# Kernel optimization log

Measured on AMD Instinct MI355X. Metric: run time of the kernel, lower is better.

The kernel has to match this reference:

```python
import jax, jax.numpy as jnp
import numpy as np

TOP_K = 2
ROUTE_SCALE = 1.0
EPS = 1e-20

B, S, D = 2, 512, 1024
E = 8            # num_experts
F = 768          # moe_intermediate_size
FS = 768 * 1     # shared expert intermediate (moe_intermediate_size * num_shared_experts)


def setup_inputs() -> dict:
    key = jax.random.key(0)
    ks = jax.random.split(key, 9)
    s = 0.02
    return {
        "hidden_states": jax.random.normal(ks[0], (B, S, D), dtype=jnp.float32),
        "W_gate_router": jax.random.normal(ks[1], (D, E), dtype=jnp.float32) * s,
        "expert_bias": jnp.zeros((E,), dtype=jnp.float32),
        "Wg": jax.random.normal(ks[2], (E, D, F), dtype=jnp.float32) * s,
        "Wu": jax.random.normal(ks[3], (E, D, F), dtype=jnp.float32) * s,
        "Wd": jax.random.normal(ks[4], (E, F, D), dtype=jnp.float32) * s,
        "Wg_s": jax.random.normal(ks[5], (D, FS), dtype=jnp.float32) * s,
        "Wu_s": jax.random.normal(ks[6], (D, FS), dtype=jnp.float32) * s,
        "Wd_s": jax.random.normal(ks[7], (FS, D), dtype=jnp.float32) * s,
    }


def reference(hidden_states, W_gate_router, expert_bias, Wg, Wu, Wd, Wg_s, Wu_s, Wd_s):
    b, s, d = hidden_states.shape
    x = hidden_states.reshape(-1, d)                      # [T, D]
    T = x.shape[0]

    # ---- token-choice top-k router (sigmoid scoring, route_norm) ----
    logits = x @ W_gate_router                            # [T, E]
    scores = jax.nn.sigmoid(logits.astype(jnp.float32))   # [T, E] fp32
    _, sel = jax.lax.top_k(scores + expert_bias, TOP_K)   # [T, K] (bias only for selection)
    top_scores = jnp.take_along_axis(scores, sel, axis=1)  # [T, K]
    top_scores = top_scores / (top_scores.sum(-1, keepdims=True) + EPS)  # route_norm
    top_scores = top_scores * ROUTE_SCALE

    # ---- shared expert (always active) ----
    shared = (jax.nn.silu(x @ Wg_s) * (x @ Wu_s)) @ Wd_s  # [T, D]

    # ---- dispatch: N = T*K routed slots (scatter-add is order-independent,
    #      so the torch stable-argsort grouping is mathematically a no-op) ----
    tok = jnp.repeat(jnp.arange(T), TOP_K)                # [N] source token per slot
    exp = sel.reshape(-1)                                 # [N] expert per slot
    w = top_scores.reshape(-1)                            # [N]
    xr = x[tok]                                           # [N, D]

    # per-expert SiLU-GLU MLP, vectorized over experts then select own expert's row
    h = jax.nn.silu(jnp.einsum('nd,edf->enf', xr, Wg)) * jnp.einsum('nd,edf->enf', xr, Wu)
    out_all = jnp.einsum('enf,efd->end', h, Wd)           # [E, N, D]
    routed = out_all[exp, jnp.arange(exp.shape[0])]       # [N, D]
    routed = (routed.astype(jnp.float32) * w[:, None]).astype(hidden_states.dtype)

    # ---- combine: scatter-add routed outputs onto shared output ----
    out = shared.at[tok].add(routed)                      # [T, D]
    return out.reshape(b, s, d)
```

## Files before the change

kernel.cpp:

```cpp
#include <hip/hip_runtime.h>
#include <hip/hip_bf16.h>
#include <math.h>

#define T_TOK   1024
#define D_DIM   1024
#define E_NUM   8
#define F_DIM   768
#define N_SLOTS 2048

typedef unsigned short u16;
typedef __attribute__((ext_vector_type(8))) short bf16x8;
typedef __attribute__((ext_vector_type(4))) float f32x4;

#define WS_SEL    0
#define WS_WTS    8192
#define WS_BUCKET 16384
#define WS_COUNTS 49152
#define WS_OFFS   49216
#define WS_POS    49280
#define WS_XB     65536
#define WS_P1     (WS_XB + 2097152)
#define WS_H      (WS_P1 + 9437184)
#define WS_WDT    (WS_H + 4718592)
#define WS_WDST   (WS_WDT + 12582912)
#define WS_WGUT   (WS_WDST + 1572864)
#define WS_WGUST  (WS_WGUT + 25165824)
#define WS_Y      WS_WGUT

__device__ __forceinline__ u16 f2bf(float x) {
    unsigned int u = __float_as_uint(x);
    u += 0x7fffu + ((u >> 16) & 1u);
    return (u16)(u >> 16);
}
__device__ __forceinline__ float bf2f(u16 h) {
    return __uint_as_float(((unsigned int)h) << 16);
}

__device__ __forceinline__ void async16(const void* g, void* s) {
    __builtin_amdgcn_global_load_lds(
        (const __attribute__((address_space(1))) unsigned int*)g,
        (__attribute__((address_space(3))) unsigned int*)s, 16, 0, 0);
}

#define PIN()   __builtin_amdgcn_sched_barrier(0)
#define BAR()   do { PIN(); __builtin_amdgcn_s_barrier(); PIN(); } while (0)
#define WAIT6() do { asm volatile("s_waitcnt vmcnt(6)" ::: "memory"); PIN(); } while (0)
#define WAIT0() do { asm volatile("s_waitcnt vmcnt(0)" ::: "memory"); PIN(); } while (0)

__global__ __launch_bounds__(256) void router_kernel(
    const float* __restrict__ X, const float* __restrict__ Wr,
    const float* __restrict__ bias, int* __restrict__ sel, float* __restrict__ wts)
{
    int t = blockIdx.x * 4 + (threadIdx.x >> 6);
    int lane = threadIdx.x & 63;
    if (t >= T_TOK) return;
    const float* xrow = X + (size_t)t * D_DIM;
    float acc[E_NUM];
#pragma unroll
    for (int e = 0; e < E_NUM; ++e) acc[e] = 0.f;
    for (int d = lane; d < D_DIM; d += 64) {
        float xv = xrow[d];
        const float4* wr = (const float4*)(Wr + (size_t)d * E_NUM);
        float4 w0 = wr[0], w1 = wr[1];
        acc[0] += xv * w0.x; acc[1] += xv * w0.y; acc[2] += xv * w0.z; acc[3] += xv * w0.w;
        acc[4] += xv * w1.x; acc[5] += xv * w1.y; acc[6] += xv * w1.z; acc[7] += xv * w1.w;
    }
#pragma unroll
    for (int e = 0; e < E_NUM; ++e)
#pragma unroll
        for (int off = 32; off > 0; off >>= 1)
            acc[e] += __shfl_xor(acc[e], off);
    if (lane == 0) {
        float s[E_NUM], b[E_NUM];
#pragma unroll
        for (int e = 0; e < E_NUM; ++e) {
            s[e] = 1.f / (1.f + expf(-acc[e]));
            b[e] = s[e] + bias[e];
        }
        int i1 = 0; float b1 = b[0];
#pragma unroll
        for (int e = 1; e < E_NUM; ++e) if (b[e] > b1) { b1 = b[e]; i1 = e; }
        int i2 = -1; float b2 = -INFINITY;
#pragma unroll
        for (int e = 0; e < E_NUM; ++e) {
            if (e == i1) continue;
            if (b[e] > b2) { b2 = b[e]; i2 = e; }
        }
        float s1 = s[i1], s2 = s[i2];
        float denom = s1 + s2 + 1e-20f;
        sel[2 * t] = i1; sel[2 * t + 1] = i2;
        wts[2 * t] = s1 / denom; wts[2 * t + 1] = s2 / denom;
    }
}

__global__ __launch_bounds__(512) void dispatch_kernel(
    const int* __restrict__ sel, int* __restrict__ bucket,
    int* __restrict__ counts, int* __restrict__ offs, int* __restrict__ pos)
{
    __shared__ int soffs[E_NUM + 1];
    int e = threadIdx.x >> 6;
    int lane = threadIdx.x & 63;
    int running = 0;
    for (int base = 0; base < N_SLOTS; base += 64) {
        int slot = base + lane;
        bool mine = (sel[slot] == e);
        unsigned long long mask = __ballot(mine);
        if (mine) {
            int rank = running + __popcll(mask & ((1ull << lane) - 1ull));
            bucket[e * T_TOK + rank] = slot;
        }
        running += __popcll(mask);
    }
    if (lane == 0) counts[e] = running;
    __syncthreads();
    if (threadIdx.x == 0) {
        int o = 0;
        for (int k = 0; k < E_NUM; ++k) { soffs[k] = o; offs[k] = o; o += counts[k]; }
        soffs[E_NUM] = o; offs[E_NUM] = o;
    }
    __syncthreads();
    int base_off = soffs[e];
    for (int r = lane; r < running; r += 64)
        pos[bucket[e * T_TOK + r]] = base_off + r;
}

__global__ __launch_bounds__(256) void transpose_cvt(
    const float* __restrict__ Wg, const float* __restrict__ Wu,
    const float* __restrict__ Wd, const float* __restrict__ Wgs,
    const float* __restrict__ Wus, const float* __restrict__ Wds,
    u16* __restrict__ Wgut, u16* __restrict__ Wdt,
    u16* __restrict__ Wgust, u16* __restrict__ Wdst)
{
    int z = blockIdx.z;
    const float* src; u16* dst; int R, C;
    if (z < 8)       { src = Wg + (size_t)z * D_DIM * F_DIM;        dst = Wgut + (size_t)z * 1536 * D_DIM;               R = D_DIM; C = F_DIM; }
    else if (z < 16) { int e = z - 8;  src = Wu + (size_t)e * D_DIM * F_DIM; dst = Wgut + (size_t)e * 1536 * D_DIM + (size_t)F_DIM * D_DIM; R = D_DIM; C = F_DIM; }
    else if (z < 24) { int e = z - 16; src = Wd + (size_t)e * F_DIM * D_DIM; dst = Wdt + (size_t)e * D_DIM * F_DIM;      R = F_DIM; C = D_DIM; }
    else if (z == 24){ src = Wgs; dst = Wgust;                      R = D_DIM; C = F_DIM; }
    else if (z == 25){ src = Wus; dst = Wgust + (size_t)F_DIM * D_DIM; R = D_DIM; C = F_DIM; }
    else             { src = Wds; dst = Wdst;                       R = F_DIM; C = D_DIM; }
    int c0 = blockIdx.x * 64, r0 = blockIdx.y * 64;
    if (c0 >= C || r0 >= R) return;

    __shared__ u16 tile[64][72];
    int t = threadIdx.x;
    int rr = t >> 4, cq = (t & 15) * 4;
#pragma unroll
    for (int i = 0; i < 4; ++i) {
        int rl = rr + 16 * i;
        float4 v = *(const float4*)(src + (size_t)(r0 + rl) * C + c0 + cq);
        tile[cq + 0][rl] = f2bf(v.x);
        tile[cq + 1][rl] = f2bf(v.y);
        tile[cq + 2][rl] = f2bf(v.z);
        tile[cq + 3][rl] = f2bf(v.w);
    }
    __syncthreads();
#pragma unroll
    for (int j = 0; j < 2; ++j) {
        int idx = t + 256 * j;
        int cc = idx >> 3, q = idx & 7;
        *(uint4*)(dst + (size_t)(c0 + cc) * R + r0 + q * 8) = *(const uint4*)&tile[cc][q * 8];
    }
}

__global__ __launch_bounds__(256) void xcvt_kernel(
    const float* __restrict__ X, u16* __restrict__ Xb)
{
    int i8 = (blockIdx.x * 256 + threadIdx.x) * 8;
    float4 v0 = *(const float4*)(X + i8);
    float4 v1 = *(const float4*)(X + i8 + 4);
    u16 o[8];
    o[0] = f2bf(v0.x); o[1] = f2bf(v0.y); o[2] = f2bf(v0.z); o[3] = f2bf(v0.w);
    o[4] = f2bf(v1.x); o[5] = f2bf(v1.y); o[6] = f2bf(v1.z); o[7] = f2bf(v1.w);
    *(uint4*)(Xb + i8) = *(const uint4*)o;
}

__global__ __launch_bounds__(256, 3) void proj1(
    const u16* __restrict__ Xb, const u16* __restrict__ Wgut, const u16* __restrict__ Wgust,
    u16* __restrict__ P1,
    const int* __restrict__ bucket, const int* __restrict__ counts, const int* __restrict__ offs)
{
    const int i = blockIdx.x;
    const int cxcd = i & 7, m = i >> 3;
    const int y = m & 15, phi = m >> 4;
    const int panel = phi * 8 + cxcd;
    const int unit = panel / 24, x = panel - unit * 24;

    int nrows, rbase; const u16* Wt;
    if (unit < E_NUM) {
        nrows = counts[unit]; rbase = offs[unit];
        Wt = Wgut + (size_t)unit * 1536 * D_DIM;
    } else {
        nrows = T_TOK; rbase = N_SLOTS; Wt = Wgust;
    }
    const int row0 = y * 128, n0 = x * 64;
    if (row0 >= nrows) return;

    __shared__ u16 smem[2][192 * 64];

    const int t = threadIdx.x;
    const int wv = t >> 6, lane = t & 63, l15 = lane & 15, lg = lane >> 4;
    const int wm = wv >> 1, wn = wv & 1;
    const int rl = lane >> 3, cch = lane & 7;

    const u16* srcA[4];
#pragma unroll
    for (int j = 0; j < 4; ++j) {
        int arow = wv * 32 + j * 8 + rl;
        int grow = min(row0 + arow, nrows - 1);
        if (unit < E_NUM) grow = bucket[unit * T_TOK + grow] >> 1;
        srcA[j] = Xb + (size_t)grow * D_DIM + (cch ^ (arow & 7)) * 8;
    }
    const u16* srcB[2];
#pragma unroll
    for (int j = 0; j < 2; ++j) {
        int brow = wv * 16 + j * 8 + rl;
        srcB[j] = Wt + (size_t)(n0 + brow) * D_DIM + (cch ^ (brow & 7)) * 8;
    }

    f32x4 acc[4][2];
    const f32x4 z4 = {0.f, 0.f, 0.f, 0.f};
#pragma unroll
    for (int ri = 0; ri < 4; ++ri)
#pragma unroll
        for (int ci = 0; ci < 2; ++ci) acc[ri][ci] = z4;

#define STAGE1(buf, kt) do { \
    _Pragma("unroll") \
    for (int j = 0; j < 4; ++j) \
        async16(srcA[j] + (kt), &smem[buf][(wv * 32 + j * 8) * 64]); \
    _Pragma("unroll") \
    for (int j = 0; j < 2; ++j) \
        async16(srcB[j] + (kt), &smem[buf][(128 + wv * 16 + j * 8) * 64]); \
} while (0)

#define COMP1(buf) do { \
    bf16x8 av[4][2], bv[2][2]; \
    _Pragma("unroll") \
    for (int ri = 0; ri < 4; ++ri) { \
        int row = wm * 64 + ri * 16 + l15; \
        _Pragma("unroll") \
        for (int kk = 0; kk < 2; ++kk) { \
            int ch = ((kk << 2) | lg) ^ (row & 7); \
            av[ri][kk] = *(const bf16x8*)&smem[buf][row * 64 + ch * 8]; \
        } \
    } \
    _Pragma("unroll") \
    for (int ci = 0; ci < 2; ++ci) { \
        int br = wn * 32 + ci * 16 + l15; \
        _Pragma("unroll") \
        for (int kk = 0; kk < 2; ++kk) { \
            int ch = ((kk << 2) | lg) ^ (br & 7); \
            bv[ci][kk] = *(const bf16x8*)&smem[buf][(128 + br) * 64 + ch * 8]; \
        } \
    } \
    _Pragma("unroll") \
    for (int kk = 0; kk < 2; ++kk) \
        _Pragma("unroll") \
        for (int ri = 0; ri < 4; ++ri) \
            _Pragma("unroll") \
            for (int ci = 0; ci < 2; ++ci) \
                acc[ri][ci] = __builtin_amdgcn_mfma_f32_16x16x32_bf16( \
                    av[ri][kk], bv[ci][kk], acc[ri][ci], 0, 0, 0); \
} while (0)

    STAGE1(0, 0);
    for (int tt = 0; tt < 16; tt += 2) {
        STAGE1(1, (tt + 1) * 64);
        WAIT6();
        BAR();
        COMP1(0);
        BAR();
        if (tt + 2 < 16) { STAGE1(0, (tt + 2) * 64); WAIT6(); }
        else             { WAIT0(); }
        BAR();
        COMP1(1);
        BAR();
    }
#undef STAGE1
#undef COMP1

#pragma unroll
    for (int ri = 0; ri < 4; ++ri)
#pragma unroll
        for (int ci = 0; ci < 2; ++ci) {
            int n = n0 + wn * 32 + ci * 16 + l15;
#pragma unroll
            for (int r = 0; r < 4; ++r) {
                int row = row0 + wm * 64 + ri * 16 + lg * 4 + r;
                if (row >= nrows) continue;
                P1[(size_t)(rbase + row) * 1536 + n] = f2bf(acc[ri][ci][r]);
            }
        }
}

__global__ __launch_bounds__(256) void glu_kernel(
    const u16* __restrict__ P1, u16* __restrict__ H)
{
    int i8 = (blockIdx.x * 256 + threadIdx.x) * 8;
    int r = i8 / F_DIM, f = i8 - r * F_DIM;
    bf16x8 g8 = *(const bf16x8*)(P1 + (size_t)r * 1536 + f);
    bf16x8 u8 = *(const bf16x8*)(P1 + (size_t)r * 1536 + F_DIM + f);
    u16 hv[8];
#pragma unroll
    for (int j = 0; j < 8; ++j) {
        float gv = bf2f((u16)g8[j]);
        float uv = bf2f((u16)u8[j]);
        hv[j] = f2bf(gv / (1.f + __expf(-gv)) * uv);
    }
    *(uint4*)(H + (size_t)r * F_DIM + f) = *(const uint4*)hv;
}

__global__ __launch_bounds__(256, 3) void proj2(
    const u16* __restrict__ H, const u16* __restrict__ Wdt, const u16* __restrict__ Wdst,
    float* __restrict__ Y,
    const int* __restrict__ counts, const int* __restrict__ offs)
{
    const int i = blockIdx.x;
    const int cxcd = i & 7, m = i >> 3;
    const int y = m & 15, phi = m >> 4;
    const int panel = phi * 8 + cxcd;
    const int unit = panel >> 4, x = panel & 15;

    int nrows, rbase; const u16* Wt;
    if (unit < E_NUM) {
        nrows = counts[unit]; rbase = offs[unit];
        Wt = Wdt + (size_t)unit * D_DIM * F_DIM;
    } else {
        nrows = T_TOK; rbase = N_SLOTS; Wt = Wdst;
    }
    const int row0 = y * 128, n0 = x * 64;
    if (row0 >= nrows) return;

    __shared__ u16 smem[2][192 * 64];

    const int t = threadIdx.x;
    const int wv = t >> 6, lane = t & 63, l15 = lane & 15, lg = lane >> 4;
    const int wm = wv >> 1, wn = wv & 1;
    const int rl = lane >> 3, cch = lane & 7;

    const u16* srcA[4];
#pragma unroll
    for (int j = 0; j < 4; ++j) {
        int arow = wv * 32 + j * 8 + rl;
        int grow = rbase + min(row0 + arow, nrows - 1);
        srcA[j] = H + (size_t)grow * F_DIM + (cch ^ (arow & 7)) * 8;
    }
    const u16* srcB[2];
#pragma unroll
    for (int j = 0; j < 2; ++j) {
        int brow = wv * 16 + j * 8 + rl;
        srcB[j] = Wt + (size_t)(n0 + brow) * F_DIM + (cch ^ (brow & 7)) * 8;
    }

    f32x4 acc[4][2];
    const f32x4 z4 = {0.f, 0.f, 0.f, 0.f};
#pragma unroll
    for (int ri = 0; ri < 4; ++ri)
#pragma unroll
        for (int ci = 0; ci < 2; ++ci) acc[ri][ci] = z4;

#define STAGE2(buf, kt) do { \
    _Pragma("unroll") \
    for (int j = 0; j < 4; ++j) \
        async16(srcA[j] + (kt), &smem[buf][(wv * 32 + j * 8) * 64]); \
    _Pragma("unroll") \
    for (int j = 0; j < 2; ++j) \
        async16(srcB[j] + (kt), &smem[buf][(128 + wv * 16 + j * 8) * 64]); \
} while (0)

#define COMP2(buf) do { \
    bf16x8 av[4][2], bv[2][2]; \
    _Pragma("unroll") \
    for (int ri = 0; ri < 4; ++ri) { \
        int row = wm * 64 + ri * 16 + l15; \
        _Pragma("unroll") \
        for (int kk = 0; kk < 2; ++kk) { \
            int ch = ((kk << 2) | lg) ^ (row & 7); \
            av[ri][kk] = *(const bf16x8*)&smem[buf][row * 64 + ch * 8]; \
        } \
    } \
    _Pragma("unroll") \
    for (int ci = 0; ci < 2; ++ci) { \
        int br = wn * 32 + ci * 16 + l15; \
        _Pragma("unroll") \
        for (int kk = 0; kk < 2; ++kk) { \
            int ch = ((kk << 2) | lg) ^ (br & 7); \
            bv[ci][kk] = *(const bf16x8*)&smem[buf][(128 + br) * 64 + ch * 8]; \
        } \
    } \
    _Pragma("unroll") \
    for (int kk = 0; kk < 2; ++kk) \
        _Pragma("unroll") \
        for (int ri = 0; ri < 4; ++ri) \
            _Pragma("unroll") \
            for (int ci = 0; ci < 2; ++ci) \
                acc[ri][ci] = __builtin_amdgcn_mfma_f32_16x16x32_bf16( \
                    av[ri][kk], bv[ci][kk], acc[ri][ci], 0, 0, 0); \
} while (0)

    STAGE2(0, 0);
    for (int tt = 0; tt < 12; tt += 2) {
        STAGE2(1, (tt + 1) * 64);
        WAIT6();
        BAR();
        COMP2(0);
        BAR();
        if (tt + 2 < 12) { STAGE2(0, (tt + 2) * 64); WAIT6(); }
        else             { WAIT0(); }
        BAR();
        COMP2(1);
        BAR();
    }
#undef STAGE2
#undef COMP2

#pragma unroll
    for (int ri = 0; ri < 4; ++ri)
#pragma unroll
        for (int ci = 0; ci < 2; ++ci) {
            int n = n0 + wn * 32 + ci * 16 + l15;
#pragma unroll
            for (int r = 0; r < 4; ++r) {
                int row = row0 + wm * 64 + ri * 16 + lg * 4 + r;
                if (row >= nrows) continue;
                Y[(size_t)(rbase + row) * D_DIM + n] = acc[ri][ci][r];
            }
        }
}

__global__ __launch_bounds__(256) void combine_kernel(
    const float* __restrict__ Y, const int* __restrict__ pos,
    const float* __restrict__ wts, float* __restrict__ out)
{
    int t = blockIdx.x;
    int d = threadIdx.x * 4;
    int p0 = pos[2 * t], p1 = pos[2 * t + 1];
    float w0 = wts[2 * t], w1 = wts[2 * t + 1];
    float4 a = *(const float4*)(Y + (size_t)(N_SLOTS + t) * D_DIM + d);
    float4 b = *(const float4*)(Y + (size_t)p0 * D_DIM + d);
    float4 cc = *(const float4*)(Y + (size_t)p1 * D_DIM + d);
    float4 o;
    o.x = a.x + w0 * b.x + w1 * cc.x;
    o.y = a.y + w0 * b.y + w1 * cc.y;
    o.z = a.z + w0 * b.z + w1 * cc.z;
    o.w = a.w + w0 * b.w + w1 * cc.w;
    *(float4*)(out + (size_t)t * D_DIM + d) = o;
}

extern "C" void kernel_launch(void* const* d_in, const int* in_sizes, int n_in,
                              void* d_out, int out_size, void* d_ws, size_t ws_size,
                              hipStream_t stream) {
    const float* X    = (const float*)d_in[0];
    const float* Wr   = (const float*)d_in[1];
    const float* bias = (const float*)d_in[2];
    const float* Wg   = (const float*)d_in[3];
    const float* Wu   = (const float*)d_in[4];
    const float* Wd   = (const float*)d_in[5];
    const float* Wgs  = (const float*)d_in[6];
    const float* Wus  = (const float*)d_in[7];
    const float* Wds  = (const float*)d_in[8];
    float* out = (float*)d_out;

    char* ws = (char*)d_ws;
    int*   sel    = (int*)(ws + WS_SEL);
    float* wtsv   = (float*)(ws + WS_WTS);
    int*   bucket = (int*)(ws + WS_BUCKET);
    int*   counts = (int*)(ws + WS_COUNTS);
    int*   offs   = (int*)(ws + WS_OFFS);
    int*   pos    = (int*)(ws + WS_POS);
    u16*   Xb     = (u16*)(ws + WS_XB);
    u16*   P1     = (u16*)(ws + WS_P1);
    u16*   H      = (u16*)(ws + WS_H);
    u16*   Wdt    = (u16*)(ws + WS_WDT);
    u16*   Wdst   = (u16*)(ws + WS_WDST);
    u16*   Wgut   = (u16*)(ws + WS_WGUT);
    u16*   Wgust  = (u16*)(ws + WS_WGUST);
    float* Y      = (float*)(ws + WS_Y);

    transpose_cvt<<<dim3(16, 16, 27), 256, 0, stream>>>(
        Wg, Wu, Wd, Wgs, Wus, Wds, Wgut, Wdt, Wgust, Wdst);
    xcvt_kernel<<<T_TOK * D_DIM / 8 / 256, 256, 0, stream>>>(X, Xb);
    router_kernel<<<256, 256, 0, stream>>>(X, Wr, bias, sel, wtsv);
    dispatch_kernel<<<1, 512, 0, stream>>>(sel, bucket, counts, offs, pos);

    proj1<<<3456, 256, 0, stream>>>(Xb, Wgut, Wgust, P1, bucket, counts, offs);
    glu_kernel<<<3072 * F_DIM / 8 / 256, 256, 0, stream>>>(P1, H);
    proj2<<<2304, 256, 0, stream>>>(H, Wdt, Wdst, Y, counts, offs);
    combine_kernel<<<T_TOK, 256, 0, stream>>>(Y, pos, wtsv, out);
}
```

Measured before the change: 99.74 us.

## Fuse SiLU-GLU into gate/up GEMM epilogue and merge x-cast into router

The bf16 conversion of x now happens inside the router kernel, so one launch replaces two. The separate GLU pass is removed: proj1 tiles the gate and up weight rows together so each block computes matching gate and up accumulators and writes silu(g)*u straight to H, dropping the P1 intermediate and its round trip. Both projection GEMMs change tile shape to 64 rows, with 128 weight columns in proj2. The grid remapping and the smaller M tiles may change reuse and occupancy.

```diff
diff --git a/kernel.cpp b/kernel.cpp
--- a/kernel.cpp
+++ b/kernel.cpp
@@ -19,8 +19,7 @@
 #define WS_OFFS   49216
 #define WS_POS    49280
 #define WS_XB     65536
-#define WS_P1     (WS_XB + 2097152)
-#define WS_H      (WS_P1 + 9437184)
+#define WS_H      (WS_XB + 2097152)
 #define WS_WDT    (WS_H + 4718592)
 #define WS_WDST   (WS_WDT + 12582912)
 #define WS_WGUT   (WS_WDST + 1572864)
@@ -47,23 +46,35 @@
 #define WAIT6() do { asm volatile("s_waitcnt vmcnt(6)" ::: "memory"); PIN(); } while (0)
 #define WAIT0() do { asm volatile("s_waitcnt vmcnt(0)" ::: "memory"); PIN(); } while (0)
 
-__global__ __launch_bounds__(256) void router_kernel(
+__global__ __launch_bounds__(256) void xrouter_kernel(
     const float* __restrict__ X, const float* __restrict__ Wr,
-    const float* __restrict__ bias, int* __restrict__ sel, float* __restrict__ wts)
+    const float* __restrict__ bias, u16* __restrict__ Xb,
+    int* __restrict__ sel, float* __restrict__ wts)
 {
     int t = blockIdx.x * 4 + (threadIdx.x >> 6);
     int lane = threadIdx.x & 63;
-    if (t >= T_TOK) return;
     const float* xrow = X + (size_t)t * D_DIM;
+    u16* brow = Xb + (size_t)t * D_DIM;
     float acc[E_NUM];
 #pragma unroll
     for (int e = 0; e < E_NUM; ++e) acc[e] = 0.f;
-    for (int d = lane; d < D_DIM; d += 64) {
-        float xv = xrow[d];
-        const float4* wr = (const float4*)(Wr + (size_t)d * E_NUM);
-        float4 w0 = wr[0], w1 = wr[1];
-        acc[0] += xv * w0.x; acc[1] += xv * w0.y; acc[2] += xv * w0.z; acc[3] += xv * w0.w;
-        acc[4] += xv * w1.x; acc[5] += xv * w1.y; acc[6] += xv * w1.z; acc[7] += xv * w1.w;
+#pragma unroll
+    for (int q = 0; q < 4; ++q) {
+        int d = q * 256 + lane * 4;
+        float4 v = *(const float4*)(xrow + d);
+        ushort4 o;
+        o.x = f2bf(v.x); o.y = f2bf(v.y); o.z = f2bf(v.z); o.w = f2bf(v.w);
+        *(ushort4*)(brow + d) = o;
+        const float xv[4] = {v.x, v.y, v.z, v.w};
+#pragma unroll
+        for (int jj = 0; jj < 4; ++jj) {
+            const float4* wr = (const float4*)(Wr + (size_t)(d + jj) * E_NUM);
+            float4 w0 = wr[0], w1 = wr[1];
+            acc[0] += xv[jj] * w0.x; acc[1] += xv[jj] * w0.y;
+            acc[2] += xv[jj] * w0.z; acc[3] += xv[jj] * w0.w;
+            acc[4] += xv[jj] * w1.x; acc[5] += xv[jj] * w1.y;
+            acc[6] += xv[jj] * w1.z; acc[7] += xv[jj] * w1.w;
+        }
     }
 #pragma unroll
     for (int e = 0; e < E_NUM; ++e)
@@ -163,28 +174,17 @@
     }
 }
 
-__global__ __launch_bounds__(256) void xcvt_kernel(
-    const float* __restrict__ X, u16* __restrict__ Xb)
-{
-    int i8 = (blockIdx.x * 256 + threadIdx.x) * 8;
-    float4 v0 = *(const float4*)(X + i8);
-    float4 v1 = *(const float4*)(X + i8 + 4);
-    u16 o[8];
-    o[0] = f2bf(v0.x); o[1] = f2bf(v0.y); o[2] = f2bf(v0.z); o[3] = f2bf(v0.w);
-    o[4] = f2bf(v1.x); o[5] = f2bf(v1.y); o[6] = f2bf(v1.z); o[7] = f2bf(v1.w);
-    *(uint4*)(Xb + i8) = *(const uint4*)o;
-}
-
 __global__ __launch_bounds__(256, 3) void proj1(
     const u16* __restrict__ Xb, const u16* __restrict__ Wgut, const u16* __restrict__ Wgust,
-    u16* __restrict__ P1,
+    u16* __restrict__ H,
     const int* __restrict__ bucket, const int* __restrict__ counts, const int* __restrict__ offs)
 {
     const int i = blockIdx.x;
     const int cxcd = i & 7, m = i >> 3;
-    const int y = m & 15, phi = m >> 4;
+    const int y = m & 31, phi = m >> 5;
     const int panel = phi * 8 + cxcd;
-    const int unit = panel / 24, x = panel - unit * 24;
+    if (panel >= 108) return;
+    const int unit = panel / 12, x = panel - unit * 12;
 
     int nrows, rbase; const u16* Wt;
     if (unit < E_NUM) {
@@ -193,7 +193,7 @@
     } else {
         nrows = T_TOK; rbase = N_SLOTS; Wt = Wgust;
     }
-    const int row0 = y * 128, n0 = x * 64;
+    const int row0 = y * 64;
     if (row0 >= nrows) return;
 
     __shared__ u16 smem[2][192 * 64];
@@ -203,42 +203,43 @@
     const int wm = wv >> 1, wn = wv & 1;
     const int rl = lane >> 3, cch = lane & 7;
 
-    const u16* srcA[4];
-#pragma unroll
-    for (int j = 0; j < 4; ++j) {
-        int arow = wv * 32 + j * 8 + rl;
+    const u16* srcA[2];
+#pragma unroll
+    for (int j = 0; j < 2; ++j) {
+        int arow = wv * 16 + j * 8 + rl;
         int grow = min(row0 + arow, nrows - 1);
         if (unit < E_NUM) grow = bucket[unit * T_TOK + grow] >> 1;
         srcA[j] = Xb + (size_t)grow * D_DIM + (cch ^ (arow & 7)) * 8;
     }
-    const u16* srcB[2];
-#pragma unroll
-    for (int j = 0; j < 2; ++j) {
-        int brow = wv * 16 + j * 8 + rl;
-        srcB[j] = Wt + (size_t)(n0 + brow) * D_DIM + (cch ^ (brow & 7)) * 8;
-    }
-
-    f32x4 acc[4][2];
+    const u16* srcB[4];
+#pragma unroll
+    for (int j = 0; j < 4; ++j) {
+        int br = wv * 32 + j * 8 + rl;
+        size_t n = (size_t)(br >> 6) * F_DIM + x * 64 + (br & 63);
+        srcB[j] = Wt + n * D_DIM + (cch ^ (br & 7)) * 8;
+    }
+
+    f32x4 accg[2][2], accu[2][2];
     const f32x4 z4 = {0.f, 0.f, 0.f, 0.f};
 #pragma unroll
-    for (int ri = 0; ri < 4; ++ri)
-#pragma unroll
-        for (int ci = 0; ci < 2; ++ci) acc[ri][ci] = z4;
+    for (int ri = 0; ri < 2; ++ri)
+#pragma unroll
+        for (int ci = 0; ci < 2; ++ci) { accg[ri][ci] = z4; accu[ri][ci] = z4; }
 
 #define STAGE1(buf, kt) do { \
     _Pragma("unroll") \
+    for (int j = 0; j < 2; ++j) \
+        async16(srcA[j] + (kt), &smem[buf][(wv * 16 + j * 8) * 64]); \
+    _Pragma("unroll") \
     for (int j = 0; j < 4; ++j) \
-        async16(srcA[j] + (kt), &smem[buf][(wv * 32 + j * 8) * 64]); \
-    _Pragma("unroll") \
-    for (int j = 0; j < 2; ++j) \
-        async16(srcB[j] + (kt), &smem[buf][(128 + wv * 16 + j * 8) * 64]); \
+        async16(srcB[j] + (kt), &smem[buf][(64 + wv * 32 + j * 8) * 64]); \
 } while (0)
 
 #define COMP1(buf) do { \
-    bf16x8 av[4][2], bv[2][2]; \
-    _Pragma("unroll") \
-    for (int ri = 0; ri < 4; ++ri) { \
-        int row = wm * 64 + ri * 16 + l15; \
+    bf16x8 av[2][2], bg[2][2], bu[2][2]; \
+    _Pragma("unroll") \
+    for (int ri = 0; ri < 2; ++ri) { \
+        int row = wm * 32 + ri * 16 + l15; \
         _Pragma("unroll") \
         for (int kk = 0; kk < 2; ++kk) { \
             int ch = ((kk << 2) | lg) ^ (row & 7); \
@@ -251,17 +252,21 @@
         _Pragma("unroll") \
         for (int kk = 0; kk < 2; ++kk) { \
             int ch = ((kk << 2) | lg) ^ (br & 7); \
-            bv[ci][kk] = *(const bf16x8*)&smem[buf][(128 + br) * 64 + ch * 8]; \
+            bg[ci][kk] = *(const bf16x8*)&smem[buf][(64 + br) * 64 + ch * 8]; \
+            bu[ci][kk] = *(const bf16x8*)&smem[buf][(128 + br) * 64 + ch * 8]; \
         } \
     } \
     _Pragma("unroll") \
     for (int kk = 0; kk < 2; ++kk) \
         _Pragma("unroll") \
-        for (int ri = 0; ri < 4; ++ri) \
+        for (int ri = 0; ri < 2; ++ri) \
             _Pragma("unroll") \
-            for (int ci = 0; ci < 2; ++ci) \
-                acc[ri][ci] = __builtin_amdgcn_mfma_f32_16x16x32_bf16( \
-                    av[ri][kk], bv[ci][kk], acc[ri][ci], 0, 0, 0); \
+            for (int ci = 0; ci < 2; ++ci) { \
+                accg[ri][ci] = __builtin_amdgcn_mfma_f32_16x16x32_bf16( \
+                    av[ri][kk], bg[ci][kk], accg[ri][ci], 0, 0, 0); \
+                accu[ri][ci] = __builtin_amdgcn_mfma_f32_16x16x32_bf16( \
+                    av[ri][kk], bu[ci][kk], accu[ri][ci], 0, 0, 0); \
+            } \
 } while (0)
 
     STAGE1(0, 0);
@@ -281,34 +286,20 @@
 #undef COMP1
 
 #pragma unroll
-    for (int ri = 0; ri < 4; ++ri)
+    for (int ri = 0; ri < 2; ++ri)
 #pragma unroll
         for (int ci = 0; ci < 2; ++ci) {
-            int n = n0 + wn * 32 + ci * 16 + l15;
+            int n = x * 64 + wn * 32 + ci * 16 + l15;
 #pragma unroll
             for (int r = 0; r < 4; ++r) {
-                int row = row0 + wm * 64 + ri * 16 + lg * 4 + r;
+                int row = row0 + wm * 32 + ri * 16 + lg * 4 + r;
                 if (row >= nrows) continue;
-                P1[(size_t)(rbase + row) * 1536 + n] = f2bf(acc[ri][ci][r]);
+                float gv = accg[ri][ci][r];
+                float uv = accu[ri][ci][r];
+                H[(size_t)(rbase + row) * F_DIM + n] =
+                    f2bf(gv / (1.f + __expf(-gv)) * uv);
             }
         }
-}
-
-__global__ __launch_bounds__(256) void glu_kernel(
-    const u16* __restrict__ P1, u16* __restrict__ H)
-{
-    int i8 = (blockIdx.x * 256 + threadIdx.x) * 8;
-    int r = i8 / F_DIM, f = i8 - r * F_DIM;
-    bf16x8 g8 = *(const bf16x8*)(P1 + (size_t)r * 1536 + f);
-    bf16x8 u8 = *(const bf16x8*)(P1 + (size_t)r * 1536 + F_DIM + f);
-    u16 hv[8];
-#pragma unroll
-    for (int j = 0; j < 8; ++j) {
-        float gv = bf2f((u16)g8[j]);
-        float uv = bf2f((u16)u8[j]);
-        hv[j] = f2bf(gv / (1.f + __expf(-gv)) * uv);
-    }
-    *(uint4*)(H + (size_t)r * F_DIM + f) = *(const uint4*)hv;
 }
 
 __global__ __launch_bounds__(256, 3) void proj2(
@@ -318,9 +309,9 @@
 {
     const int i = blockIdx.x;
     const int cxcd = i & 7, m = i >> 3;
-    const int y = m & 15, phi = m >> 4;
+    const int y = m & 31, phi = m >> 5;
     const int panel = phi * 8 + cxcd;
-    const int unit = panel >> 4, x = panel & 15;
+    const int unit = panel >> 3, x = panel & 7;
 
     int nrows, rbase; const u16* Wt;
     if (unit < E_NUM) {
@@ -329,7 +320,7 @@
     } else {
         nrows = T_TOK; rbase = N_SLOTS; Wt = Wdst;
     }
-    const int row0 = y * 128, n0 = x * 64;
+    const int row0 = y * 64, n0 = x * 128;
     if (row0 >= nrows) return;
 
     __shared__ u16 smem[2][192 * 64];
@@ -339,41 +330,41 @@
     const int wm = wv >> 1, wn = wv & 1;
     const int rl = lane >> 3, cch = lane & 7;
 
-    const u16* srcA[4];
-#pragma unroll
-    for (int j = 0; j < 4; ++j) {
-        int arow = wv * 32 + j * 8 + rl;
+    const u16* srcA[2];
+#pragma unroll
+    for (int j = 0; j < 2; ++j) {
+        int arow = wv * 16 + j * 8 + rl;
         int grow = rbase + min(row0 + arow, nrows - 1);
         srcA[j] = H + (size_t)grow * F_DIM + (cch ^ (arow & 7)) * 8;
     }
-    const u16* srcB[2];
-#pragma unroll
-    for (int j = 0; j < 2; ++j) {
-        int brow = wv * 16 + j * 8 + rl;
-        srcB[j] = Wt + (size_t)(n0 + brow) * F_DIM + (cch ^ (brow & 7)) * 8;
-    }
-
-    f32x4 acc[4][2];
+    const u16* srcB[4];
+#pragma unroll
+    for (int j = 0; j < 4; ++j) {
+        int br = wv * 32 + j * 8 + rl;
+        srcB[j] = Wt + (size_t)(n0 + br) * F_DIM + (cch ^ (br & 7)) * 8;
+    }
+
+    f32x4 acc[2][4];
     const f32x4 z4 = {0.f, 0.f, 0.f, 0.f};
 #pragma unroll
-    for (int ri = 0; ri < 4; ++ri)
-#pragma unroll
-        for (int ci = 0; ci < 2; ++ci) acc[ri][ci] = z4;
+    for (int ri = 0; ri < 2; ++ri)
+#pragma unroll
+        for (int ci = 0; ci < 4; ++ci) acc[ri][ci] = z4;
 
 #define STAGE2(buf, kt) do { \
     _Pragma("unroll") \
+    for (int j = 0; j < 2; ++j) \
+        async16(srcA[j] + (kt), &smem[buf][(wv * 16 + j * 8) * 64]); \
+    _Pragma("unroll") \
     for (int j = 0; j < 4; ++j) \
-        async16(srcA[j] + (kt), &smem[buf][(wv * 32 + j * 8) * 64]); \
-    _Pragma("unroll") \
-    for (int j = 0; j < 2; ++j) \
-        async16(srcB[j] + (kt), &smem[buf][(128 + wv * 16 + j * 8) * 64]); \
+        async16(srcB[j] + (kt), &smem[buf][(64 + wv * 32 + j * 8) * 64]); \
 } while (0)
 
 #define COMP2(buf) do { \
-    bf16x8 av[4][2], bv[2][2]; \
-    _Pragma("unroll") \
-    for (int ri = 0; ri < 4; ++ri) { \
-        int row = wm * 64 + ri * 16 + l15; \
+    bf16x8 av[2][2], bv[4][2]; \
+    _Pragma("unroll") \
+    for (int ri = 0; ri < 2; ++ri) { \
+        int row = wm * 32 + ri * 16 + l15; \
         _Pragma("unroll") \
         for (int kk = 0; kk < 2; ++kk) { \
             int ch = ((kk << 2) | lg) ^ (row & 7); \
@@ -381,20 +372,20 @@
         } \
     } \
     _Pragma("unroll") \
-    for (int ci = 0; ci < 2; ++ci) { \
-        int br = wn * 32 + ci * 16 + l15; \
+    for (int ci = 0; ci < 4; ++ci) { \
+        int br = wn * 64 + ci * 16 + l15; \
         _Pragma("unroll") \
         for (int kk = 0; kk < 2; ++kk) { \
             int ch = ((kk << 2) | lg) ^ (br & 7); \
-            bv[ci][kk] = *(const bf16x8*)&smem[buf][(128 + br) * 64 + ch * 8]; \
+            bv[ci][kk] = *(const bf16x8*)&smem[buf][(64 + br) * 64 + ch * 8]; \
         } \
     } \
     _Pragma("unroll") \
     for (int kk = 0; kk < 2; ++kk) \
         _Pragma("unroll") \
-        for (int ri = 0; ri < 4; ++ri) \
+        for (int ri = 0; ri < 2; ++ri) \
             _Pragma("unroll") \
-            for (int ci = 0; ci < 2; ++ci) \
+            for (int ci = 0; ci < 4; ++ci) \
                 acc[ri][ci] = __builtin_amdgcn_mfma_f32_16x16x32_bf16( \
                     av[ri][kk], bv[ci][kk], acc[ri][ci], 0, 0, 0); \
 } while (0)
@@ -416,13 +407,13 @@
 #undef COMP2
 
 #pragma unroll
-    for (int ri = 0; ri < 4; ++ri)
-#pragma unroll
-        for (int ci = 0; ci < 2; ++ci) {
-            int n = n0 + wn * 32 + ci * 16 + l15;
+    for (int ri = 0; ri < 2; ++ri)
+#pragma unroll
+        for (int ci = 0; ci < 4; ++ci) {
+            int n = n0 + wn * 64 + ci * 16 + l15;
 #pragma unroll
             for (int r = 0; r < 4; ++r) {
-                int row = row0 + wm * 64 + ri * 16 + lg * 4 + r;
+                int row = row0 + wm * 32 + ri * 16 + lg * 4 + r;
                 if (row >= nrows) continue;
                 Y[(size_t)(rbase + row) * D_DIM + n] = acc[ri][ci][r];
             }
@@ -470,7 +461,6 @@
     int*   offs   = (int*)(ws + WS_OFFS);
     int*   pos    = (int*)(ws + WS_POS);
     u16*   Xb     = (u16*)(ws + WS_XB);
-    u16*   P1     = (u16*)(ws + WS_P1);
     u16*   H      = (u16*)(ws + WS_H);
     u16*   Wdt    = (u16*)(ws + WS_WDT);
     u16*   Wdst   = (u16*)(ws + WS_WDST);
@@ -478,14 +468,12 @@
     u16*   Wgust  = (u16*)(ws + WS_WGUST);
     float* Y      = (float*)(ws + WS_Y);
 
+    xrouter_kernel<<<256, 256, 0, stream>>>(X, Wr, bias, Xb, sel, wtsv);
+    dispatch_kernel<<<1, 512, 0, stream>>>(sel, bucket, counts, offs, pos);
     transpose_cvt<<<dim3(16, 16, 27), 256, 0, stream>>>(
         Wg, Wu, Wd, Wgs, Wus, Wds, Wgut, Wdt, Wgust, Wdst);
-    xcvt_kernel<<<T_TOK * D_DIM / 8 / 256, 256, 0, stream>>>(X, Xb);
-    router_kernel<<<256, 256, 0, stream>>>(X, Wr, bias, sel, wtsv);
-    dispatch_kernel<<<1, 512, 0, stream>>>(sel, bucket, counts, offs, pos);
-
-    proj1<<<3456, 256, 0, stream>>>(Xb, Wgut, Wgust, P1, bucket, counts, offs);
-    glu_kernel<<<3072 * F_DIM / 8 / 256, 256, 0, stream>>>(P1, H);
+
+    proj1<<<3584, 256, 0, stream>>>(Xb, Wgut, Wgust, H, bucket, counts, offs);
     proj2<<<2304, 256, 0, stream>>>(H, Wdt, Wdst, Y, counts, offs);
     combine_kernel<<<T_TOK, 256, 0, stream>>>(Y, pos, wtsv, out);
 }
```

Result: faster. 85.31 us (-14.5%).
